# Kernel tuning notes

Measured on AMD Instinct MI355X. Metric: run time of the kernel, lower is better.

## Reference

```python
import jax, jax.numpy as jnp
import numpy as np

BN_EPS = 1e-5

def batchnorm(x, gamma, beta):
    # training-mode BatchNorm1d over the row (node/sample) dimension
    mu = jnp.mean(x, axis=0)
    var = jnp.var(x, axis=0)
    return (x - mu) * jax.lax.rsqrt(var + BN_EPS) * gamma + beta

def gin_mean(h, src, dst, n):
    # DGL GINConv(apply_func=None, aggregator='mean', eps=0):
    # h_new = h + mean_{u in N(v)} h_u
    ones = jnp.ones((src.shape[0],), h.dtype)
    deg = jax.ops.segment_sum(ones, dst, num_segments=n)
    agg = jax.ops.segment_sum(h[src], dst, num_segments=n)
    return h + agg / jnp.maximum(deg, 1.0)[:, None]

def setup_inputs() -> dict:
    key = jax.random.key(0)
    ks = jax.random.split(key, 12)
    N, E, B, K = 10000, 160000, 64, 10
    DIN, D, DH = 20, 512, 256
    x = jax.random.normal(ks[0], (N, DIN), dtype=jnp.float32)
    edge_src = jax.random.randint(ks[1], (E,), 0, N, dtype=jnp.int32)
    edge_dst = jax.random.randint(ks[2], (E,), 0, N, dtype=jnp.int32)
    node2graph = jnp.sort(jax.random.randint(ks[3], (N,), 0, B, dtype=jnp.int32))
    pg_emb = jax.random.normal(ks[4], (B, D), dtype=jnp.float32)
    neigh_emb = jax.random.normal(ks[5], (B, K, D), dtype=jnp.float32)
    s = lambda i, shp: jax.random.normal(ks[i], shp, dtype=jnp.float32) * 0.02
    return dict(
        x=x, pg_emb=pg_emb, neigh_emb=neigh_emb,
        W_init=s(6, (DIN, D)), b_init=jnp.zeros((D,), jnp.float32),
        g1=jnp.ones((D,), jnp.float32), be1=jnp.zeros((D,), jnp.float32),
        g2=jnp.ones((D,), jnp.float32), be2=jnp.zeros((D,), jnp.float32),
        W_fc=s(7, (3 * D, DH)), b_fc=jnp.zeros((DH,), jnp.float32),
        W_fc2=s(8, (DH, DH)), b_fc2=jnp.zeros((DH,), jnp.float32),
        W_fc3=s(9, (DH, DH)), b_fc3=jnp.zeros((DH,), jnp.float32),
        W_fc4=s(10, (DH, 1)), b_fc4=jnp.zeros((1,), jnp.float32),
        gb=jnp.ones((DH,), jnp.float32), bb=jnp.zeros((DH,), jnp.float32),
        gb2=jnp.ones((DH,), jnp.float32), bb2=jnp.zeros((DH,), jnp.float32),
        gb3=jnp.ones((DH,), jnp.float32), bb3=jnp.zeros((DH,), jnp.float32),
        edge_src=edge_src, edge_dst=edge_dst, node2graph=node2graph,
    )

def reference(x, pg_emb, neigh_emb, W_init, b_init, g1, be1, g2, be2,
              W_fc, b_fc, W_fc2, b_fc2, W_fc3, b_fc3, W_fc4, b_fc4,
              gb, bb, gb2, bb2, gb3, bb3, edge_src, edge_dst, node2graph):
    N = x.shape[0]
    B, K, D = neigh_emb.shape
    # two GIN(mean) layers with BN+ReLU on the batched graph
    h = x @ W_init + b_init                                   # [N, 512]
    h = jax.nn.relu(batchnorm(gin_mean(h, edge_src, edge_dst, N), g1, be1))
    h = jax.nn.relu(batchnorm(gin_mean(h, edge_src, edge_dst, N), g2, be2))
    # dgl.mean_nodes: per-graph mean readout
    cnt = jax.ops.segment_sum(jnp.ones((N,), h.dtype), node2graph, num_segments=B)
    qemb = jax.ops.segment_sum(h, node2graph, num_segments=B) / jnp.maximum(cnt, 1.0)[:, None]
    a = jnp.concatenate([qemb, pg_emb], axis=1)               # [B, 2D]
    a = jnp.broadcast_to(a[:, None, :], (B, K, 2 * D))        # repeat per candidate
    b = jnp.concatenate([a, neigh_emb], axis=-1).reshape(B * K, 3 * D)
    H = jax.nn.relu(batchnorm(b @ W_fc + b_fc, gb, bb))
    H2 = jax.nn.relu(batchnorm(H @ W_fc2 + b_fc2, gb2, bb2))
    H3 = jax.nn.relu(batchnorm(H2 @ W_fc3 + b_fc3, gb3, bb3))
    pred = jax.nn.sigmoid(H3 @ W_fc4 + b_fc4)                 # [B*K, 1]
    return pred.reshape(B, K)
```

## Files before the change

kernel.cpp:

```cpp
#include <hip/hip_runtime.h>
#include <hip/hip_bf16.h>
#include <math.h>

#define N_NODES 10000
#define N_EDGES 160000
#define D 512
#define DIN 20
#define B 64
#define KC 10
#define DH 256
#define NROW (B*KC)
#define BN_EPS 1e-5f

#define ZCOUNT 36356
#define Z4 (ZCOUNT/4)
#define D4 (N_NODES/4)
#define IM_ROWS 8
#define IM_UNITS (N_NODES/IM_ROWS)
#define DEG_BLOCKS 625
#define GWAVES 4
#define GBLOCKS 625
#define F1_NS 6
#define F1_ROWS 8
#define F1_KS 256
#define TB 160

struct P {
  const float *x, *pg, *neigh, *Winit, *binit;
  const float *g1, *be1, *g2, *be2;
  const float *Wfc, *bfc, *W2, *b2, *W3, *b3, *W4, *b4;
  const float *gbA, *bbA, *gbB, *bbB, *gbC, *bbC;
  const int *esrc, *edst, *n2g;
  unsigned short *hb0, *hb1, *hb2;
  float *zbuf, *csum1, *csq1, *csum2, *csq2;
  float *s1,*q1,*s2,*q2,*s3,*q3, *qemb;
  int *bar;
  float *G1,*G2,*G3,*part;
  int *degi,*rowstart,*cursor,*csr,*gstart;
  float *out;
};

__device__ __forceinline__ void f4acc(float4& a, const float4 v){
  a.x += v.x; a.y += v.y; a.z += v.z; a.w += v.w;
}
__device__ __forceinline__ void mk_affine(const float4 s, const float4 q, const float4 g,
                                          const float4 b, float4& sc, float4& sh){
  const float invN = 1.0f/(float)N_NODES;
  float mu, var, rs;
  mu = s.x*invN; var = q.x*invN - mu*mu; rs = rsqrtf(var+BN_EPS); sc.x = rs*g.x; sh.x = b.x - mu*sc.x;
  mu = s.y*invN; var = q.y*invN - mu*mu; rs = rsqrtf(var+BN_EPS); sc.y = rs*g.y; sh.y = b.y - mu*sc.y;
  mu = s.z*invN; var = q.z*invN - mu*mu; rs = rsqrtf(var+BN_EPS); sc.z = rs*g.z; sh.z = b.z - mu*sc.z;
  mu = s.w*invN; var = q.w*invN - mu*mu; rs = rsqrtf(var+BN_EPS); sc.w = rs*g.w; sh.w = b.w - mu*sc.w;
}
__device__ __forceinline__ float4 aff_relu(const float4 v, const float4 sc, const float4 sh){
  float4 o;
  o.x = fmaxf(fmaf(v.x, sc.x, sh.x), 0.0f);
  o.y = fmaxf(fmaf(v.y, sc.y, sh.y), 0.0f);
  o.z = fmaxf(fmaf(v.z, sc.z, sh.z), 0.0f);
  o.w = fmaxf(fmaf(v.w, sc.w, sh.w), 0.0f);
  return o;
}
__device__ __forceinline__ void bf_unpack(const uint4 u, float4& lo, float4& hi){
  lo.x = __uint_as_float(u.x << 16); lo.y = __uint_as_float(u.x & 0xffff0000u);
  lo.z = __uint_as_float(u.y << 16); lo.w = __uint_as_float(u.y & 0xffff0000u);
  hi.x = __uint_as_float(u.z << 16); hi.y = __uint_as_float(u.z & 0xffff0000u);
  hi.z = __uint_as_float(u.w << 16); hi.w = __uint_as_float(u.w & 0xffff0000u);
}
__device__ __forceinline__ unsigned bf_pack2(float a, float b){
  unsigned ua = __float_as_uint(a); ua = (ua + 0x7fffu + ((ua>>16)&1u)) >> 16;
  unsigned ub = __float_as_uint(b); ub = (ub + 0x7fffu + ((ub>>16)&1u)) & 0xffff0000u;
  return (ua & 0xffffu) | ub;
}
__device__ __forceinline__ unsigned short bf_pack1(float a){
  unsigned ua = __float_as_uint(a); return (unsigned short)((ua + 0x7fffu + ((ua>>16)&1u)) >> 16);
}

template<bool FUSED>
__device__ __forceinline__ void gather_body(const P& p,
    const unsigned short* __restrict__ hin, unsigned short* __restrict__ hout,
    const float* pcs, const float* pcq, const float* pgm, const float* pbt,
    float* cs, float* cq, float* red){
  int t = threadIdx.x;
  int lane = t & 63;
  int wave = t >> 6;
  int wid  = blockIdx.x*GWAVES + wave;
  int tot  = gridDim.x*GWAVES;
  const uint4* hb4 = (const uint4*)hin;
  float4 scA, shA, scB, shB;
  if (FUSED){
    mk_affine(((const float4*)pcs)[2*lane],   ((const float4*)pcq)[2*lane],
              ((const float4*)pgm)[2*lane],   ((const float4*)pbt)[2*lane],   scA, shA);
    mk_affine(((const float4*)pcs)[2*lane+1], ((const float4*)pcq)[2*lane+1],
              ((const float4*)pgm)[2*lane+1], ((const float4*)pbt)[2*lane+1], scB, shB);
  }
  float4 sLo = make_float4(0,0,0,0), sHi = make_float4(0,0,0,0);
  float4 qLo = make_float4(0,0,0,0), qHi = make_float4(0,0,0,0);
  for (int node = wid; node < N_NODES; node += tot){
    int start = p.rowstart[node], end = p.rowstart[node+1];
    float4 aLo = make_float4(0,0,0,0), aHi = make_float4(0,0,0,0);
    float4 bLo = make_float4(0,0,0,0), bHi = make_float4(0,0,0,0);
    for (int base = start; base < end; base += 64){
      int cnt = end - base; if (cnt > 64) cnt = 64;
      int myidx = (lane < cnt) ? p.csr[base+lane] : 0;
      int j = 0;
      for (; j+8 <= cnt; j += 8){
        uint4 u[8];
        #pragma unroll
        for (int k = 0; k < 8; ++k){
          int idx = __shfl(myidx, j+k, 64);
          u[k] = hb4[(size_t)idx*64 + lane];
        }
        #pragma unroll
        for (int k = 0; k < 8; ++k){
          float4 lo, hi; bf_unpack(u[k], lo, hi);
          if (FUSED){ lo = aff_relu(lo, scA, shA); hi = aff_relu(hi, scB, shB); }
          if (k & 1){ f4acc(bLo, lo); f4acc(bHi, hi); }
          else      { f4acc(aLo, lo); f4acc(aHi, hi); }
        }
      }
      for (; j < cnt; ++j){
        int idx = __shfl(myidx, j, 64);
        uint4 u0 = hb4[(size_t)idx*64 + lane];
        float4 lo, hi; bf_unpack(u0, lo, hi);
        if (FUSED){ lo = aff_relu(lo, scA, shA); hi = aff_relu(hi, scB, shB); }
        f4acc(aLo, lo); f4acc(aHi, hi);
      }
    }
    float inv = 1.0f/fmaxf((float)(end-start), 1.0f);
    uint4 us = hb4[(size_t)node*64 + lane];
    float4 hLo, hHi; bf_unpack(us, hLo, hHi);
    if (FUSED){ hLo = aff_relu(hLo, scA, shA); hHi = aff_relu(hHi, scB, shB); }
    float4 oLo, oHi;
    oLo.x = hLo.x + (aLo.x+bLo.x)*inv;  oLo.y = hLo.y + (aLo.y+bLo.y)*inv;
    oLo.z = hLo.z + (aLo.z+bLo.z)*inv;  oLo.w = hLo.w + (aLo.w+bLo.w)*inv;
    oHi.x = hHi.x + (aHi.x+bHi.x)*inv;  oHi.y = hHi.y + (aHi.y+bHi.y)*inv;
    oHi.z = hHi.z + (aHi.z+bHi.z)*inv;  oHi.w = hHi.w + (aHi.w+bHi.w)*inv;
    uint4 ou;
    ou.x = bf_pack2(oLo.x, oLo.y); ou.y = bf_pack2(oLo.z, oLo.w);
    ou.z = bf_pack2(oHi.x, oHi.y); ou.w = bf_pack2(oHi.z, oHi.w);
    ((uint4*)hout)[(size_t)node*64 + lane] = ou;
    f4acc(sLo, oLo); f4acc(sHi, oHi);
    qLo.x += oLo.x*oLo.x; qLo.y += oLo.y*oLo.y; qLo.z += oLo.z*oLo.z; qLo.w += oLo.w*oLo.w;
    qHi.x += oHi.x*oHi.x; qHi.y += oHi.y*oHi.y; qHi.z += oHi.z*oHi.z; qHi.w += oHi.w*oHi.w;
  }
  float* my = red + wave*1024;
  int c = 8*lane;
  *((float4*)&my[c])      = sLo;  *((float4*)&my[c+4])     = sHi;
  *((float4*)&my[512+c])  = qLo;  *((float4*)&my[512+c+4]) = qHi;
  __syncthreads();
  for (int e = t; e < 1024; e += 256){
    float v = red[e] + red[1024+e] + red[2048+e] + red[3072+e];
    if (e < 512) atomicAdd(&cs[e], v);
    else         atomicAdd(&cq[e-512], v);
  }
}

__global__ __launch_bounds__(256) void k_setup(P p){
  int b = blockIdx.x, nb = gridDim.x, t = threadIdx.x;
  for (int i4 = b*256 + t; i4 < Z4 + D4; i4 += nb*256){
    if (i4 < Z4) ((float4*)p.zbuf)[i4] = make_float4(0.f,0.f,0.f,0.f);
    else         ((int4*)p.degi)[i4 - Z4] = make_int4(0,0,0,0);
  }
  if (b == 0 && t <= B){
    int lo = 0, hi = N_NODES;
    while (lo < hi){ int mid = (lo+hi)>>1; if (p.n2g[mid] < t) lo = mid+1; else hi = mid; }
    p.gstart[t] = lo;
  }
}

__global__ __launch_bounds__(256) void k_deg_init(P p){
  __shared__ float xs[IM_ROWS*DIN];
  int t = threadIdx.x;
  if (blockIdx.x < DEG_BLOCKS){
    int e = blockIdx.x*256 + t;
    if (e < N_EDGES) atomicAdd(&p.degi[p.edst[e]], 1);
    return;
  }
  int unit = blockIdx.x - DEG_BLOCKS;
  float wlo[DIN], whi[DIN];
  #pragma unroll
  for (int k = 0; k < DIN; ++k){ wlo[k] = p.Winit[k*D + t]; whi[k] = p.Winit[k*D + t + 256]; }
  float b0 = p.binit[t], b1 = p.binit[t+256];
  int r0 = unit*IM_ROWS;
  for (int i = t; i < IM_ROWS*DIN; i += 256) xs[i] = p.x[(size_t)r0*DIN + i];
  __syncthreads();
  for (int rr = 0; rr < IM_ROWS; ++rr){
    float a0 = b0, a1 = b1;
    #pragma unroll
    for (int k = 0; k < DIN; ++k){
      float xv = xs[rr*DIN + k];
      a0 += xv*wlo[k]; a1 += xv*whi[k];
    }
    p.hb0[(size_t)(r0+rr)*D + t]       = bf_pack1(a0);
    p.hb0[(size_t)(r0+rr)*D + t + 256] = bf_pack1(a1);
  }
}

__global__ __launch_bounds__(256) void k_scan(P p){
  __shared__ int part[256];
  int t = threadIdx.x;
  const int PER = (N_NODES + 255)/256;
  int base = t*PER;
  int s = 0;
  for (int i = 0; i < PER; ++i){ int idx = base+i; if (idx < N_NODES) s += p.degi[idx]; }
  part[t] = s;
  __syncthreads();
  for (int off = 1; off < 256; off <<= 1){
    int v = (t >= off) ? part[t-off] : 0;
    __syncthreads();
    part[t] += v;
    __syncthreads();
  }
  int run = (t > 0) ? part[t-1] : 0;
  for (int i = 0; i < PER; ++i){
    int idx = base+i;
    if (idx < N_NODES){ p.rowstart[idx] = run; p.cursor[idx] = run; run += p.degi[idx]; }
  }
  if (t == 255) p.rowstart[N_NODES] = run;
}

__global__ __launch_bounds__(256) void k_fill(P p){
  int e = blockIdx.x*256 + threadIdx.x;
  if (e < N_EDGES){
    int pos = atomicAdd(&p.cursor[p.edst[e]], 1);
    p.csr[pos] = p.esrc[e];
  }
}

__global__ __launch_bounds__(256) void k_g1(P p){
  __shared__ float red[4096];
  gather_body<false>(p, p.hb0, p.hb1, nullptr,nullptr,nullptr,nullptr, p.csum1, p.csq1, red);
}
__global__ __launch_bounds__(256) void k_g2(P p){
  __shared__ float red[4096];
  gather_body<true>(p, p.hb1, p.hb2, p.csum1, p.csq1, p.g1, p.be1, p.csum2, p.csq2, red);
}

__global__ __launch_bounds__(256) void k_readout(P p){
  __shared__ float red[2048];
  int g = blockIdx.x >> 3, chunk = blockIdx.x & 7;
  int t = threadIdx.x;
  int lane = t & 63, wave = t >> 6;
  const uint4* hb4 = (const uint4*)p.hb2;
  float4 scA, shA, scB, shB;
  mk_affine(((const float4*)p.csum2)[2*lane],   ((const float4*)p.csq2)[2*lane],
            ((const float4*)p.g2)[2*lane],      ((const float4*)p.be2)[2*lane],   scA, shA);
  mk_affine(((const float4*)p.csum2)[2*lane+1], ((const float4*)p.csq2)[2*lane+1],
            ((const float4*)p.g2)[2*lane+1],    ((const float4*)p.be2)[2*lane+1], scB, shB);
  int s = p.gstart[g], e = p.gstart[g+1];
  int rows = e - s;
  int per = (rows + 7)/8;
  int r0 = s + chunk*per;
  int r1 = r0 + per; if (r1 > e) r1 = e;
  float4 aLo = make_float4(0,0,0,0), aHi = make_float4(0,0,0,0);
  for (int r = r0 + wave; r < r1; r += 4){
    uint4 u = hb4[(size_t)r*64 + lane];
    float4 lo, hi; bf_unpack(u, lo, hi);
    lo = aff_relu(lo, scA, shA); hi = aff_relu(hi, scB, shB);
    f4acc(aLo, lo); f4acc(aHi, hi);
  }
  int c = 8*lane;
  *((float4*)&red[wave*512 + c])     = aLo;
  *((float4*)&red[wave*512 + c + 4]) = aHi;
  __syncthreads();
  for (int e2 = t; e2 < 512; e2 += 256){
    float v = red[e2] + red[512+e2] + red[1024+e2] + red[1536+e2];
    atomicAdd(&p.qemb[(size_t)g*D + e2], v);
  }
}

__global__ __launch_bounds__(256) void k_fc1(P p){
  __shared__ float brow[F1_ROWS*F1_KS];
  int t = threadIdx.x;
  int rb = blockIdx.x % 80, ks = blockIdx.x / 80;
  int r0 = rb*F1_ROWS, k0 = ks*F1_KS;
  for (int rr = 0; rr < F1_ROWS; ++rr){
    int r = r0+rr;
    int g = r/KC, k = r - g*KC;
    int j = k0 + t;
    float v;
    if (j < D){
      float invc = 1.0f/fmaxf((float)(p.gstart[g+1]-p.gstart[g]), 1.0f);
      v = p.qemb[(size_t)g*D + j]*invc;
    } else if (j < 2*D){
      v = p.pg[(size_t)g*D + (j-D)];
    } else {
      v = p.neigh[((size_t)g*KC + k)*D + (j-2*D)];
    }
    brow[rr*F1_KS + t] = v;
  }
  __syncthreads();
  float acc[F1_ROWS] = {0.f,0.f,0.f,0.f,0.f,0.f,0.f,0.f};
  #pragma unroll 4
  for (int kk = 0; kk < F1_KS; ++kk){
    float w = p.Wfc[(size_t)(k0+kk)*DH + t];
    #pragma unroll
    for (int rr = 0; rr < F1_ROWS; ++rr) acc[rr] += brow[rr*F1_KS + kk]*w;
  }
  for (int rr = 0; rr < F1_ROWS; ++rr)
    p.part[((size_t)ks*NROW + r0+rr)*DH + t] = acc[rr];
}

__device__ __forceinline__ void grid_bar(int* cnt, int target){
  __syncthreads();
  if (threadIdx.x == 0){
    atomicAdd(cnt, 1);
    while (atomicAdd(cnt, 0) < target) ;
  }
  __syncthreads();
}

__device__ __forceinline__ void fc_layer(const float* in, const float* ps, const float* pq,
    const float* gamma, const float* beta, const float* W, const float* bias,
    float* outG, float* s, float* q, int b, int t, float* row){
  int r0 = b*4;
  const float invM = 1.0f/(float)NROW;
  #pragma unroll
  for (int i = 0; i < 4; ++i){
    int idx = t + i*256;
    int rr = idx >> 8, kk = idx & 255;
    float mu = ps[kk]*invM;
    float var = pq[kk]*invM - mu*mu;
    float rs = rsqrtf(var + BN_EPS);
    float v = in[(size_t)(r0+rr)*DH + kk];
    row[rr*DH + kk] = fmaxf((v-mu)*rs*gamma[kk] + beta[kk], 0.0f);
  }
  __syncthreads();
  float bv = bias[t];
  float a0 = bv, a1 = bv, a2 = bv, a3 = bv;
  #pragma unroll 4
  for (int kk = 0; kk < DH; ++kk){
    float w = W[(size_t)kk*DH + t];
    a0 += row[0*DH+kk]*w; a1 += row[1*DH+kk]*w;
    a2 += row[2*DH+kk]*w; a3 += row[3*DH+kk]*w;
  }
  outG[(size_t)(r0+0)*DH + t] = a0;
  outG[(size_t)(r0+1)*DH + t] = a1;
  outG[(size_t)(r0+2)*DH + t] = a2;
  outG[(size_t)(r0+3)*DH + t] = a3;
  atomicAdd(&s[t], a0+a1+a2+a3);
  atomicAdd(&q[t], a0*a0 + a1*a1 + a2*a2 + a3*a3);
  __syncthreads();
}

__global__ __launch_bounds__(256, 2) void k_tail(P p){
  __shared__ float row[4*DH];
  int t = threadIdx.x, b = blockIdx.x;
  {
    int r0 = b*4;
    float bval = p.bfc[t];
    float ls = 0.f, lq = 0.f;
    for (int rr = 0; rr < 4; ++rr){
      int r = r0+rr;
      float acc = bval;
      for (int sl = 0; sl < F1_NS; ++sl) acc += p.part[((size_t)sl*NROW + r)*DH + t];
      p.G1[(size_t)r*DH + t] = acc;
      ls += acc; lq += acc*acc;
    }
    atomicAdd(&p.s1[t], ls); atomicAdd(&p.q1[t], lq);
  }
  grid_bar(p.bar, TB);
  fc_layer(p.G1, p.s1, p.q1, p.gbA, p.bbA, p.W2, p.b2, p.G2, p.s2, p.q2, b, t, row);
  grid_bar(p.bar, 2*TB);
  fc_layer(p.G2, p.s2, p.q2, p.gbB, p.bbB, p.W3, p.b3, p.G3, p.s3, p.q3, b, t, row);
  grid_bar(p.bar, 3*TB);
  {
    int wave = t>>6, lane = t&63;
    int r = b*4 + wave;
    const float invM = 1.0f/(float)NROW;
    float sum = 0.f;
    #pragma unroll
    for (int j = 0; j < 4; ++j){
      int c = lane + 64*j;
      float mu = p.s3[c]*invM;
      float var = p.q3[c]*invM - mu*mu;
      float rs = rsqrtf(var+BN_EPS);
      float v = p.G3[(size_t)r*DH + c];
      v = fmaxf((v-mu)*rs*p.gbC[c] + p.bbC[c], 0.0f);
      sum += v*p.W4[c];
    }
    #pragma unroll
    for (int off = 32; off > 0; off >>= 1) sum += __shfl_down(sum, off, 64);
    if (lane == 0){
      float z = sum + p.b4[0];
      p.out[r] = 1.0f/(1.0f + expf(-z));
    }
  }
}

extern "C" void kernel_launch(void* const* d_in, const int* in_sizes, int n_in,
                              void* d_out, int out_size, void* d_ws, size_t ws_size,
                              hipStream_t stream) {
  P p;
  p.x     = (const float*)d_in[0];
  p.pg    = (const float*)d_in[1];
  p.neigh = (const float*)d_in[2];
  p.Winit = (const float*)d_in[3];
  p.binit = (const float*)d_in[4];
  p.g1    = (const float*)d_in[5];
  p.be1   = (const float*)d_in[6];
  p.g2    = (const float*)d_in[7];
  p.be2   = (const float*)d_in[8];
  p.Wfc   = (const float*)d_in[9];
  p.bfc   = (const float*)d_in[10];
  p.W2    = (const float*)d_in[11];
  p.b2    = (const float*)d_in[12];
  p.W3    = (const float*)d_in[13];
  p.b3    = (const float*)d_in[14];
  p.W4    = (const float*)d_in[15];
  p.b4    = (const float*)d_in[16];
  p.gbA   = (const float*)d_in[17];
  p.bbA   = (const float*)d_in[18];
  p.gbB   = (const float*)d_in[19];
  p.bbB   = (const float*)d_in[20];
  p.gbC   = (const float*)d_in[21];
  p.bbC   = (const float*)d_in[22];
  p.esrc  = (const int*)d_in[23];
  p.edst  = (const int*)d_in[24];
  p.n2g   = (const int*)d_in[25];
  p.out   = (float*)d_out;

  float* ws = (float*)d_ws;
  size_t off = 0;
  p.hb0 = (unsigned short*)(ws + off); off += (size_t)N_NODES*D/2;
  p.hb1 = (unsigned short*)(ws + off); off += (size_t)N_NODES*D/2;
  p.hb2 = (unsigned short*)(ws + off); off += (size_t)N_NODES*D/2;
  p.zbuf  = ws + off;
  p.csum1 = ws + off; off += 512;
  p.csq1  = ws + off; off += 512;
  p.csum2 = ws + off; off += 512;
  p.csq2  = ws + off; off += 512;
  p.s1    = ws + off; off += 256;
  p.q1    = ws + off; off += 256;
  p.s2    = ws + off; off += 256;
  p.q2    = ws + off; off += 256;
  p.s3    = ws + off; off += 256;
  p.q3    = ws + off; off += 256;
  p.qemb  = ws + off; off += (size_t)B*D;
  p.bar   = (int*)(ws + off); off += 4;
  p.G1   = ws + off; off += (size_t)NROW*DH;
  p.G2   = ws + off; off += (size_t)NROW*DH;
  p.G3   = ws + off; off += (size_t)NROW*DH;
  p.part = ws + off; off += (size_t)F1_NS*NROW*DH;
  p.degi     = (int*)(ws + off); off += N_NODES;
  p.rowstart = (int*)(ws + off); off += N_NODES + 1;
  p.cursor   = (int*)(ws + off); off += N_NODES;
  p.csr      = (int*)(ws + off); off += N_EDGES;
  p.gstart   = (int*)(ws + off); off += B + 1;

  k_setup<<<64, 256, 0, stream>>>(p);
  k_deg_init<<<DEG_BLOCKS + IM_UNITS, 256, 0, stream>>>(p);
  k_scan<<<1, 256, 0, stream>>>(p);
  k_fill<<<(N_EDGES+255)/256, 256, 0, stream>>>(p);
  k_g1<<<GBLOCKS, 256, 0, stream>>>(p);
  k_g2<<<GBLOCKS, 256, 0, stream>>>(p);
  k_readout<<<512, 256, 0, stream>>>(p);
  k_fc1<<<480, 256, 0, stream>>>(p);
  k_tail<<<TB, 256, 0, stream>>>(p);
}
```

Measured before the change: 213.0 us.

## Replace persistent tail kernel grid barriers with separate kernel launches

Splits the persistent k_tail kernel, which used spin-wait atomic grid barriers, into four kernels (reduce, fc2, fc3, final), so the stream ordering does the synchronisation between layers. This removes the global atomic spinning and any risk from co-residency assumptions, at the cost of extra launch overhead for each small kernel. The BN normalisation in the FC layers is also simplified so each thread computes stats for its own column, and ZCOUNT shrinks by four now that the barrier counter is gone.

```diff
diff --git a/kernel.cpp b/kernel.cpp
--- a/kernel.cpp
+++ b/kernel.cpp
@@ -12,7 +12,7 @@
 #define NROW (B*KC)
 #define BN_EPS 1e-5f
 
-#define ZCOUNT 36356
+#define ZCOUNT 36352
 #define Z4 (ZCOUNT/4)
 #define D4 (N_NODES/4)
 #define IM_ROWS 8
@@ -23,7 +23,6 @@
 #define F1_NS 6
 #define F1_ROWS 8
 #define F1_KS 256
-#define TB 160
 
 struct P {
   const float *x, *pg, *neigh, *Winit, *binit;
@@ -34,7 +33,6 @@
   unsigned short *hb0, *hb1, *hb2;
   float *zbuf, *csum1, *csq1, *csum2, *csq2;
   float *s1,*q1,*s2,*q2,*s3,*q3, *qemb;
-  int *bar;
   float *G1,*G2,*G3,*part;
   int *degi,*rowstart,*cursor,*csr,*gstart;
   float *out;
@@ -301,38 +299,44 @@
     p.part[((size_t)ks*NROW + r0+rr)*DH + t] = acc[rr];
 }
 
-__device__ __forceinline__ void grid_bar(int* cnt, int target){
-  __syncthreads();
-  if (threadIdx.x == 0){
-    atomicAdd(cnt, 1);
-    while (atomicAdd(cnt, 0) < target) ;
-  }
-  __syncthreads();
-}
-
-__device__ __forceinline__ void fc_layer(const float* in, const float* ps, const float* pq,
+__global__ __launch_bounds__(256) void k_reduce(P p){
+  int t = threadIdx.x;
+  int r0 = blockIdx.x*8;
+  float bval = p.bfc[t];
+  float ls = 0.f, lq = 0.f;
+  #pragma unroll
+  for (int rr = 0; rr < 8; ++rr){
+    int r = r0+rr;
+    float acc = bval;
+    #pragma unroll
+    for (int sl = 0; sl < F1_NS; ++sl) acc += p.part[((size_t)sl*NROW + r)*DH + t];
+    p.G1[(size_t)r*DH + t] = acc;
+    ls += acc; lq += acc*acc;
+  }
+  atomicAdd(&p.s1[t], ls); atomicAdd(&p.q1[t], lq);
+}
+
+__device__ __forceinline__ void fcmid_full(const float* in, const float* ps, const float* pq,
     const float* gamma, const float* beta, const float* W, const float* bias,
-    float* outG, float* s, float* q, int b, int t, float* row){
-  int r0 = b*4;
+    float* outG, float* s, float* q){
+  __shared__ float nrm[4*DH];
+  int t = threadIdx.x;
+  int r0 = blockIdx.x*4;
   const float invM = 1.0f/(float)NROW;
+  float mu = ps[t]*invM;
+  float rs = rsqrtf(pq[t]*invM - mu*mu + BN_EPS);
+  float ga = gamma[t], be = beta[t];
   #pragma unroll
-  for (int i = 0; i < 4; ++i){
-    int idx = t + i*256;
-    int rr = idx >> 8, kk = idx & 255;
-    float mu = ps[kk]*invM;
-    float var = pq[kk]*invM - mu*mu;
-    float rs = rsqrtf(var + BN_EPS);
-    float v = in[(size_t)(r0+rr)*DH + kk];
-    row[rr*DH + kk] = fmaxf((v-mu)*rs*gamma[kk] + beta[kk], 0.0f);
-  }
+  for (int rr = 0; rr < 4; ++rr)
+    nrm[rr*DH + t] = fmaxf((in[(size_t)(r0+rr)*DH + t]-mu)*rs*ga + be, 0.0f);
   __syncthreads();
   float bv = bias[t];
   float a0 = bv, a1 = bv, a2 = bv, a3 = bv;
   #pragma unroll 4
   for (int kk = 0; kk < DH; ++kk){
     float w = W[(size_t)kk*DH + t];
-    a0 += row[0*DH+kk]*w; a1 += row[1*DH+kk]*w;
-    a2 += row[2*DH+kk]*w; a3 += row[3*DH+kk]*w;
+    a0 += nrm[0*DH+kk]*w; a1 += nrm[1*DH+kk]*w;
+    a2 += nrm[2*DH+kk]*w; a3 += nrm[3*DH+kk]*w;
   }
   outG[(size_t)(r0+0)*DH + t] = a0;
   outG[(size_t)(r0+1)*DH + t] = a1;
@@ -340,51 +344,34 @@
   outG[(size_t)(r0+3)*DH + t] = a3;
   atomicAdd(&s[t], a0+a1+a2+a3);
   atomicAdd(&q[t], a0*a0 + a1*a1 + a2*a2 + a3*a3);
-  __syncthreads();
-}
-
-__global__ __launch_bounds__(256, 2) void k_tail(P p){
-  __shared__ float row[4*DH];
-  int t = threadIdx.x, b = blockIdx.x;
-  {
-    int r0 = b*4;
-    float bval = p.bfc[t];
-    float ls = 0.f, lq = 0.f;
-    for (int rr = 0; rr < 4; ++rr){
-      int r = r0+rr;
-      float acc = bval;
-      for (int sl = 0; sl < F1_NS; ++sl) acc += p.part[((size_t)sl*NROW + r)*DH + t];
-      p.G1[(size_t)r*DH + t] = acc;
-      ls += acc; lq += acc*acc;
-    }
-    atomicAdd(&p.s1[t], ls); atomicAdd(&p.q1[t], lq);
-  }
-  grid_bar(p.bar, TB);
-  fc_layer(p.G1, p.s1, p.q1, p.gbA, p.bbA, p.W2, p.b2, p.G2, p.s2, p.q2, b, t, row);
-  grid_bar(p.bar, 2*TB);
-  fc_layer(p.G2, p.s2, p.q2, p.gbB, p.bbB, p.W3, p.b3, p.G3, p.s3, p.q3, b, t, row);
-  grid_bar(p.bar, 3*TB);
-  {
-    int wave = t>>6, lane = t&63;
-    int r = b*4 + wave;
-    const float invM = 1.0f/(float)NROW;
-    float sum = 0.f;
-    #pragma unroll
-    for (int j = 0; j < 4; ++j){
-      int c = lane + 64*j;
-      float mu = p.s3[c]*invM;
-      float var = p.q3[c]*invM - mu*mu;
-      float rs = rsqrtf(var+BN_EPS);
-      float v = p.G3[(size_t)r*DH + c];
-      v = fmaxf((v-mu)*rs*p.gbC[c] + p.bbC[c], 0.0f);
-      sum += v*p.W4[c];
-    }
-    #pragma unroll
-    for (int off = 32; off > 0; off >>= 1) sum += __shfl_down(sum, off, 64);
-    if (lane == 0){
-      float z = sum + p.b4[0];
-      p.out[r] = 1.0f/(1.0f + expf(-z));
-    }
+}
+__global__ __launch_bounds__(256) void k_fc2(P p){
+  fcmid_full(p.G1, p.s1, p.q1, p.gbA, p.bbA, p.W2, p.b2, p.G2, p.s2, p.q2);
+}
+__global__ __launch_bounds__(256) void k_fc3(P p){
+  fcmid_full(p.G2, p.s2, p.q2, p.gbB, p.bbB, p.W3, p.b3, p.G3, p.s3, p.q3);
+}
+
+__global__ __launch_bounds__(256) void k_final(P p){
+  int t = threadIdx.x;
+  int wave = t>>6, lane = t&63;
+  int r = blockIdx.x*4 + wave;
+  const float invM = 1.0f/(float)NROW;
+  float sum = 0.f;
+  #pragma unroll
+  for (int j = 0; j < 4; ++j){
+    int c = lane + 64*j;
+    float mu = p.s3[c]*invM;
+    float rs = rsqrtf(p.q3[c]*invM - mu*mu + BN_EPS);
+    float v = p.G3[(size_t)r*DH + c];
+    v = fmaxf((v-mu)*rs*p.gbC[c] + p.bbC[c], 0.0f);
+    sum += v*p.W4[c];
+  }
+  #pragma unroll
+  for (int off = 32; off > 0; off >>= 1) sum += __shfl_down(sum, off, 64);
+  if (lane == 0){
+    float z = sum + p.b4[0];
+    p.out[r] = 1.0f/(1.0f + expf(-z));
   }
 }
 
@@ -437,7 +424,6 @@
   p.s3    = ws + off; off += 256;
   p.q3    = ws + off; off += 256;
   p.qemb  = ws + off; off += (size_t)B*D;
-  p.bar   = (int*)(ws + off); off += 4;
   p.G1   = ws + off; off += (size_t)NROW*DH;
   p.G2   = ws + off; off += (size_t)NROW*DH;
   p.G3   = ws + off; off += (size_t)NROW*DH;
@@ -456,5 +442,8 @@
   k_g2<<<GBLOCKS, 256, 0, stream>>>(p);
   k_readout<<<512, 256, 0, stream>>>(p);
   k_fc1<<<480, 256, 0, stream>>>(p);
-  k_tail<<<TB, 256, 0, stream>>>(p);
-}
+  k_reduce<<<NROW/8, 256, 0, stream>>>(p);
+  k_fc2<<<NROW/4, 256, 0, stream>>>(p);
+  k_fc3<<<NROW/4, 256, 0, stream>>>(p);
+  k_final<<<NROW/4, 256, 0, stream>>>(p);
+}
```

Result: no change. 215.0 us (+1.0%).
